# Optimization experiments

Measured on AMD Instinct MI355X. Metric: run time of the kernel, lower is better.

Reference implementation:

```python
import jax, jax.numpy as jnp
import numpy as np

RADIUS = 1.0
NORM_ORD = 2.0
N_POINTS = 4194304


def _contract(p):
    # p: [..., 3] -> contracted points [..., 3] (MipNeRF-360 eq. 10)
    eps = jnp.finfo(p.dtype).eps
    mag = jnp.linalg.norm(p, ord=NORM_ORD, axis=-1)
    mag = jnp.maximum(mag, eps)
    norm_factor = (2.0 - RADIUS / mag) / mag
    mask = (mag <= RADIUS)[..., None]
    return jnp.where(mask, p / RADIUS, norm_factor[..., None] * p)


def setup_inputs() -> dict:
    key = jax.random.key(0)
    x = jax.random.normal(key, (N_POINTS, 3), dtype=jnp.float32) * 2.0
    return {"x": x, "output_jacobian": 1}


def reference(x, output_jacobian):
    x_contr = _contract(x)
    if output_jacobian:
        # per-point 3x3 jacobian, mirroring torch.func.vmap(jacrev(contract))
        jacobian = jax.vmap(jax.jacrev(_contract))(x.reshape(-1, x.shape[-1]))
        jacobian = jacobian.reshape(x.shape[:-1] + (x.shape[-1], x.shape[-1]))
        return (x_contr, jacobian)
    return x_contr
```

## Files before the change

kernel.cpp:

```cpp
#include <hip/hip_runtime.h>


typedef float v4f __attribute__((ext_vector_type(4)));

constexpr int BLOCK = 256;
constexpr int PPB   = 1024;

__global__ __launch_bounds__(BLOCK) void contract_jac_kernel(
    const float* __restrict__ x,
    float* __restrict__ out,
    long long n_points)
{
    __shared__ float  sp[PPB * 3];
    __shared__ float2 ssc[PPB];

    const int tid = threadIdx.x;
    const long long blk = blockIdx.x;

    const v4f* x4 = reinterpret_cast<const v4f*>(x) + blk * 768;
    v4f* sp4 = reinterpret_cast<v4f*>(sp);
    #pragma unroll
    for (int i = 0; i < 3; ++i)
        sp4[tid + i * BLOCK] = x4[tid + i * BLOCK];
    __syncthreads();

    #pragma unroll
    for (int k = 0; k < 4; ++k) {
        int q = tid + k * BLOCK;
        float px = sp[3*q + 0], py = sp[3*q + 1], pz = sp[3*q + 2];
        float m2 = fmaf(px, px, fmaf(py, py, pz * pz));
        float m  = sqrtf(m2);
        float s = 1.0f, coef = 0.0f;
        if (m > 1.0f) {
            float inv = 1.0f / m;
            s    = (2.0f - inv) * inv;
            coef = 2.0f * (1.0f - m) / (m2 * m2);
        }
        ssc[q] = make_float2(s, coef);
    }
    __syncthreads();

    float* ocb = out + blk * 3072;
    #pragma unroll
    for (int i = 0; i < 3; ++i) {
        int g = tid + i * BLOCK;
        v4f v;
        #pragma unroll
        for (int j = 0; j < 4; ++j) {
            unsigned F = 4u * g + j;
            unsigned q = F / 3u;
            v[j] = ssc[q].x * sp[F];
        }
        reinterpret_cast<v4f*>(ocb)[g] = v;
    }

    float* ojb = out + n_points * 3 + blk * 9216;
    #pragma unroll
    for (int i = 0; i < 9; ++i) {
        int g = tid + i * BLOCK;
        v4f v;
        #pragma unroll
        for (int j = 0; j < 4; ++j) {
            unsigned E = 4u * g + j;
            unsigned q = E / 9u;
            unsigned r = E - 9u * q;
            unsigned a = (r * 11u) >> 5;
            unsigned b = r - 3u * a;
            float2 sc2 = ssc[q];
            float val = sc2.y * sp[3u*q + a] * sp[3u*q + b];
            val = (a == b) ? val + sc2.x : val;
            v[j] = val;
        }
        reinterpret_cast<v4f*>(ojb)[g] = v;
    }
}

extern "C" void kernel_launch(void* const* d_in, const int* in_sizes, int n_in,
                              void* d_out, int out_size, void* d_ws, size_t ws_size,
                              hipStream_t stream) {
    const float* x = (const float*)d_in[0];
    float* out = (float*)d_out;

    long long n = in_sizes[0] / 3;
    int grid = (int)(n / PPB);

    contract_jac_kernel<<<grid, BLOCK, 0, stream>>>(x, out, n);
}
```

Before: 238.3 us.

## Drop shared-memory staging; compute four consecutive points per thread in registers

Each thread now loads three float4 vectors holding four consecutive points, computes the scale and coefficient in registers, and writes its own contracted points and jacobians directly as float4 vectors. This removes the LDS staging, both barriers, and the per-element divide/mod index arithmetic. The math also switches from sqrt and divides to rsqrt, which can change rounding slightly. Per-thread global accesses are now strided (12 and 36 floats apart across lanes), so coalescing relies on the cache and may be worse than the previous contiguous block pattern.

```diff
diff --git a/kernel.cpp b/kernel.cpp
--- a/kernel.cpp
+++ b/kernel.cpp
@@ -4,74 +4,69 @@
 typedef float v4f __attribute__((ext_vector_type(4)));
 
 constexpr int BLOCK = 256;
-constexpr int PPB   = 1024;
+constexpr int PPT   = 4;
+constexpr int PPB   = BLOCK * PPT;
 
 __global__ __launch_bounds__(BLOCK) void contract_jac_kernel(
     const float* __restrict__ x,
     float* __restrict__ out,
     long long n_points)
 {
-    __shared__ float  sp[PPB * 3];
-    __shared__ float2 ssc[PPB];
+    const long long t = (long long)blockIdx.x * BLOCK + threadIdx.x;
 
-    const int tid = threadIdx.x;
-    const long long blk = blockIdx.x;
+    const v4f* x4 = reinterpret_cast<const v4f*>(x) + 3 * t;
+    v4f a = x4[0], b = x4[1], c = x4[2];
 
-    const v4f* x4 = reinterpret_cast<const v4f*>(x) + blk * 768;
-    v4f* sp4 = reinterpret_cast<v4f*>(sp);
+    float px[PPT] = {a.x, a.w, b.z, c.y};
+    float py[PPT] = {a.y, b.x, b.w, c.z};
+    float pz[PPT] = {a.z, b.y, c.x, c.w};
+
+    float s[PPT], cf[PPT];
     #pragma unroll
-    for (int i = 0; i < 3; ++i)
-        sp4[tid + i * BLOCK] = x4[tid + i * BLOCK];
-    __syncthreads();
-
-    #pragma unroll
-    for (int k = 0; k < 4; ++k) {
-        int q = tid + k * BLOCK;
-        float px = sp[3*q + 0], py = sp[3*q + 1], pz = sp[3*q + 2];
-        float m2 = fmaf(px, px, fmaf(py, py, pz * pz));
-        float m  = sqrtf(m2);
-        float s = 1.0f, coef = 0.0f;
-        if (m > 1.0f) {
-            float inv = 1.0f / m;
-            s    = (2.0f - inv) * inv;
-            coef = 2.0f * (1.0f - m) / (m2 * m2);
-        }
-        ssc[q] = make_float2(s, coef);
-    }
-    __syncthreads();
-
-    float* ocb = out + blk * 3072;
-    #pragma unroll
-    for (int i = 0; i < 3; ++i) {
-        int g = tid + i * BLOCK;
-        v4f v;
-        #pragma unroll
-        for (int j = 0; j < 4; ++j) {
-            unsigned F = 4u * g + j;
-            unsigned q = F / 3u;
-            v[j] = ssc[q].x * sp[F];
-        }
-        reinterpret_cast<v4f*>(ocb)[g] = v;
+    for (int k = 0; k < PPT; ++k) {
+        float m2   = fmaf(px[k], px[k], fmaf(py[k], py[k], pz[k] * pz[k]));
+        float invm = rsqrtf(m2);
+        float m    = m2 * invm;
+        float sv   = (2.0f - invm) * invm;
+        float i2   = invm * invm;
+        float cv   = 2.0f * (1.0f - m) * (i2 * i2);
+        bool inside = (m2 <= 1.0f);
+        s[k]  = inside ? 1.0f : sv;
+        cf[k] = inside ? 0.0f : cv;
     }
 
-    float* ojb = out + n_points * 3 + blk * 9216;
+    v4f* oc = reinterpret_cast<v4f*>(out) + 3 * t;
+    v4f o0 = {s[0] * px[0], s[0] * py[0], s[0] * pz[0], s[1] * px[1]};
+    v4f o1 = {s[1] * py[1], s[1] * pz[1], s[2] * px[2], s[2] * py[2]};
+    v4f o2 = {s[2] * pz[2], s[3] * px[3], s[3] * py[3], s[3] * pz[3]};
+    oc[0] = o0; oc[1] = o1; oc[2] = o2;
+
+    float j[PPT * 9];
+    #pragma unroll
+    for (int k = 0; k < PPT; ++k) {
+        float cx = cf[k] * px[k];
+        float cy = cf[k] * py[k];
+        float cz = cf[k] * pz[k];
+        float xy = cx * py[k];
+        float xz = cx * pz[k];
+        float yz = cy * pz[k];
+        float* J = j + 9 * k;
+        J[0] = fmaf(cx, px[k], s[k]);
+        J[1] = xy;
+        J[2] = xz;
+        J[3] = xy;
+        J[4] = fmaf(cy, py[k], s[k]);
+        J[5] = yz;
+        J[6] = xz;
+        J[7] = yz;
+        J[8] = fmaf(cz, pz[k], s[k]);
+    }
+
+    v4f* oj = reinterpret_cast<v4f*>(out + n_points * 3) + 9 * t;
     #pragma unroll
     for (int i = 0; i < 9; ++i) {
-        int g = tid + i * BLOCK;
-        v4f v;
-        #pragma unroll
-        for (int j = 0; j < 4; ++j) {
-            unsigned E = 4u * g + j;
-            unsigned q = E / 9u;
-            unsigned r = E - 9u * q;
-            unsigned a = (r * 11u) >> 5;
-            unsigned b = r - 3u * a;
-            float2 sc2 = ssc[q];
-            float val = sc2.y * sp[3u*q + a] * sp[3u*q + b];
-            val = (a == b) ? val + sc2.x : val;
-            v[j] = val;
-        }
-        reinterpret_cast<v4f*>(ojb)[g] = v;
+        v4f v = {j[4*i + 0], j[4*i + 1], j[4*i + 2], j[4*i + 3]};
+        oj[i] = v;
     }
 }
 
```

Result: slower. 269.0 us (+12.9%).
